# Optimization experiments

Measured on AMD Instinct MI355X. Metric: run time of the kernel, lower is better.

The kernel has to match this reference:

```python
import jax, jax.numpy as jnp
import numpy as np

NUM_HEADS = 16
HEAD_DIM = 128
ROTARY_DIM = 32  # head_dim * rotary_pct(0.25)
ROPE_BASE = 10000.0
SCALE = HEAD_DIM ** -0.5


def _rotate_half(x):
    x1, x2 = jnp.split(x, 2, axis=-1)
    return jnp.concatenate((-x2, x1), axis=-1)


def _rope_tables(seq_len, dtype):
    inv_freq = 1.0 / (ROPE_BASE ** (jnp.arange(0, ROTARY_DIM, 2, dtype=jnp.float32) / ROTARY_DIM))
    freqs = jnp.arange(seq_len, dtype=jnp.float32)[:, None] * inv_freq[None, :]  # [S, rd/2]
    emb = jnp.concatenate((freqs, freqs), axis=-1)  # [S, rd]
    return jnp.cos(emb).astype(dtype), jnp.sin(emb).astype(dtype)


def setup_inputs() -> dict:
    key = jax.random.key(0)
    k1, k2, k3 = jax.random.split(key, 3)
    B, S, H = 2, 2048, 2048
    hidden_states = jax.random.normal(k1, (B, S, H), dtype=jnp.float32)
    attention_mask = jnp.zeros((B, 1, S, S), dtype=jnp.float32)
    Wqkv = jax.random.normal(k2, (H, 3 * H), dtype=jnp.float32) * (H ** -0.5)
    Wout = jax.random.normal(k3, (H, H), dtype=jnp.float32) * (H ** -0.5)
    return {"hidden_states": hidden_states, "attention_mask": attention_mask,
            "Wqkv": Wqkv, "Wout": Wout}


def reference(hidden_states, attention_mask, Wqkv, Wout):
    B, S, H = hidden_states.shape
    qkv = jnp.einsum('bsh,hk->bsk', hidden_states, Wqkv)  # [B,S,3H]
    q, k, v = jnp.split(qkv, 3, axis=-1)

    def to_heads(x):
        return x.reshape(B, S, NUM_HEADS, HEAD_DIM).transpose(0, 2, 1, 3)  # [B,nh,S,hd]

    q, k, v = to_heads(q), to_heads(k), to_heads(v)

    cos, sin = _rope_tables(S, hidden_states.dtype)  # [S, ROTARY_DIM]
    cos = cos[None, None, :, :]
    sin = sin[None, None, :, :]

    def rope(x):
        xr = x[..., :ROTARY_DIM]
        xr = xr * cos + _rotate_half(xr) * sin
        return jnp.concatenate((xr, x[..., ROTARY_DIM:]), axis=-1)

    q, k = rope(q), rope(k)

    scores = jnp.einsum('bhqd,bhkd->bhqk', q, k) * SCALE + attention_mask
    probs = jax.nn.softmax(scores, axis=-1)  # dropout p=0 -> identity
    ctx = jnp.einsum('bhqk,bhkd->bhqd', probs, v)
    ctx = ctx.transpose(0, 2, 1, 3).reshape(B, S, H)
    return jnp.einsum('bsh,ho->bso', ctx, Wout)
```

## Files before the change

### kernel.cpp

```cpp
#include <hip/hip_runtime.h>

typedef __attribute__((ext_vector_type(4))) float f32x4;
typedef __attribute__((ext_vector_type(16))) float f32x16;
typedef __attribute__((ext_vector_type(8))) short s16x8;
typedef __attribute__((ext_vector_type(4))) unsigned short u16x4;
typedef __attribute__((ext_vector_type(8))) unsigned short u16x8;

#define DEVINL __device__ __forceinline__

constexpr int Bb = 2;
constexpr int Ss = 2048;
constexpr int Hh = 2048;
constexpr int NH = 16;
constexpr int HD = 128;
constexpr float ATT_SCALE = 0.08838834764831845f;
constexpr float CEXP = ATT_SCALE * 1.44269504089f;
constexpr float INV_SCALE = 11.313708498984761f;
constexpr float RAW_THR = 90.50966799f;

DEVINL unsigned short f2bf(float f) {
    unsigned u = __float_as_uint(f);
    u += 0x7FFFu + ((u >> 16) & 1u);
    return (unsigned short)(u >> 16);
}
DEVINL float bf2f(unsigned short h) { return __uint_as_float(((unsigned)h) << 16); }
DEVINL float fexp2(float x) { return __builtin_amdgcn_exp2f(x); }

DEVINL void gl16(const void* g, void* l) {
    __builtin_amdgcn_global_load_lds((const __attribute__((address_space(1))) void*)g,
                                     (__attribute__((address_space(3))) void*)l, 16, 0, 0);
}

__global__ void scan_mask_k(const float* __restrict__ m, int* __restrict__ flag) {
    size_t i = ((size_t)blockIdx.x * 256 + threadIdx.x) * 4;
    f32x4 v = *(const f32x4*)(m + i);
    int any = (v[0] != 0.f) || (v[1] != 0.f) || (v[2] != 0.f) || (v[3] != 0.f);
    if (__any(any)) { if ((threadIdx.x & 63) == 0) atomicOr(flag, 1); }
}

__global__ void convH_k(const float* __restrict__ x, unsigned short* __restrict__ y) {
    size_t i = (size_t)blockIdx.x * 256 + threadIdx.x;
    f32x4 a = *(const f32x4*)(x + i * 8);
    f32x4 b = *(const f32x4*)(x + i * 8 + 4);
    u16x8 o;
    o[0] = f2bf(a[0]); o[1] = f2bf(a[1]); o[2] = f2bf(a[2]); o[3] = f2bf(a[3]);
    o[4] = f2bf(b[0]); o[5] = f2bf(b[1]); o[6] = f2bf(b[2]); o[7] = f2bf(b[3]);
    *(u16x8*)(y + i * 8) = o;
}

__global__ void convT_k(const float* __restrict__ W, unsigned short* __restrict__ Wt,
                        int R, int C) {
    __shared__ float tile[32][33];
    int c0 = blockIdx.x * 32, r0 = blockIdx.y * 32;
    int t = threadIdx.x;
    int rr = t >> 3, cc = (t & 7) * 4;
    f32x4 v = *(const f32x4*)(W + (size_t)(r0 + rr) * C + c0 + cc);
    tile[rr][cc + 0] = v[0]; tile[rr][cc + 1] = v[1];
    tile[rr][cc + 2] = v[2]; tile[rr][cc + 3] = v[3];
    __syncthreads();
    u16x4 o;
    o[0] = f2bf(tile[cc + 0][rr]); o[1] = f2bf(tile[cc + 1][rr]);
    o[2] = f2bf(tile[cc + 2][rr]); o[3] = f2bf(tile[cc + 3][rr]);
    *(u16x4*)(Wt + (size_t)(c0 + rr) * R + r0 + cc) = o;
}

template<int MODE>
__global__ __launch_bounds__(512, 2)
void gemm128x256_k(const unsigned short* __restrict__ A, const unsigned short* __restrict__ Bt,
                   float* __restrict__ Cf, unsigned short* __restrict__ Cb,
                   unsigned short* __restrict__ VtOut,
                   int M, int N, int K, int rm, int rn, int snx) {
    __shared__ char lds[98304];
    int t = threadIdx.x, w = t >> 6, ln = t & 63, lr = ln & 15, lg = ln >> 4;
    int wm = w >> 2, wn = w & 3;
    int f = blockIdx.x;
    int xcd = f & 7, i0 = f >> 3;
    int mb = (xcd / snx) * rm + i0 % rm;
    int nb = (xcd % snx) * rn + i0 / rm;
    int m0 = mb * 128, n0 = nb * 256;
    const char* Ab = (const char*)A;
    const char* Bbp = (const char*)Bt;

    f32x4 acc[4][4];
#pragma unroll
    for (int i = 0; i < 4; ++i)
#pragma unroll
        for (int j = 0; j < 4; ++j) { acc[i][j][0] = 0.f; acc[i][j][1] = 0.f; acc[i][j][2] = 0.f; acc[i][j][3] = 0.f; }

    auto STGA = [&](int sbuf, int skh, int kt) {
        int row = t >> 2, c = t & 3;
        int cs = c ^ ((row >> 1) & 3);
        gl16(Ab + ((size_t)(m0 + row) * K + kt * 64 + skh * 32) * 2 + cs * 16,
             lds + sbuf * 49152 + skh * 8192 + t * 16);
    };
    auto STGB = [&](int sbuf, int skh, int kt) {
#pragma unroll
        for (int rr = 0; rr < 2; ++rr) {
            int ci = rr * 512 + t;
            int row = ci >> 2, c = ci & 3;
            int cs = c ^ ((row >> 1) & 3);
            gl16(Bbp + ((size_t)(n0 + row) * K + kt * 64 + skh * 32) * 2 + cs * 16,
                 lds + sbuf * 49152 + 16384 + skh * 16384 + ci * 16);
        }
    };

#define PH128(buf, kh, sbuf, skh, st)                                             \
  {                                                                               \
    const char* Ap = lds + (buf) * 49152 + (kh) * 8192;                           \
    const char* Bp = lds + (buf) * 49152 + 16384 + (kh) * 16384;                  \
    s16x8 af[4], bfr[4];                                                          \
    _Pragma("unroll")                                                             \
    for (int i = 0; i < 4; ++i) {                                                 \
      int row = wm * 64 + i * 16 + lr;                                            \
      af[i] = *(const s16x8*)(Ap + row * 64 + ((lg ^ ((row >> 1) & 3)) * 16));    \
    }                                                                             \
    _Pragma("unroll")                                                             \
    for (int j = 0; j < 4; ++j) {                                                 \
      int row = wn * 64 + j * 16 + lr;                                            \
      bfr[j] = *(const s16x8*)(Bp + row * 64 + ((lg ^ ((row >> 1) & 3)) * 16));   \
    }                                                                             \
    STGA(sbuf, skh, st); STGB(sbuf, skh, st);                                     \
    __builtin_amdgcn_s_barrier();                                                 \
    asm volatile("s_waitcnt lgkmcnt(0)" ::: "memory");                            \
    __builtin_amdgcn_s_setprio(1);                                                \
    _Pragma("unroll")                                                             \
    for (int i = 0; i < 4; ++i)                                                   \
      _Pragma("unroll")                                                           \
      for (int j = 0; j < 4; ++j)                                                 \
        acc[i][j] = __builtin_amdgcn_mfma_f32_16x16x32_bf16(af[i], bfr[j],        \
                                                            acc[i][j], 0, 0, 0); \
    __builtin_amdgcn_s_setprio(0);                                                \
    asm volatile("s_waitcnt vmcnt(6)" ::: "memory");                              \
    __builtin_amdgcn_s_barrier();                                                 \
  }

    const int NT = K >> 6;
    STGA(0, 0, 0); STGB(0, 0, 0);
    STGA(0, 1, 0); STGB(0, 1, 0);
    STGA(1, 0, 1); STGB(1, 0, 1);
    asm volatile("s_waitcnt vmcnt(3)" ::: "memory");
    __builtin_amdgcn_s_barrier();

    for (int it = 0; it < (NT >> 1); ++it) {
        int e = it * 2;
        int e2 = (e + 2 < NT) ? e + 2 : e;
        int e3 = (e + 3 < NT) ? e + 3 : e + 1;
        PH128(0, 0,  1, 1, e + 1)
        PH128(0, 1,  0, 0, e2)
        PH128(1, 0,  0, 1, e2)
        PH128(1, 1,  1, 0, e3)
    }
    asm volatile("s_waitcnt vmcnt(0)" ::: "memory");
#undef PH128

    if (MODE == 0 && n0 >= 4096) {
#pragma unroll
        for (int i = 0; i < 4; ++i)
#pragma unroll
            for (int j = 0; j < 4; ++j) {
                int vcol = n0 - 4096 + wn * 64 + j * 16 + lr;
                int h = vcol >> 7, d = vcol & 127;
                int gr = m0 + wm * 64 + i * 16 + lg * 4;
                int bb = gr >> 11, si = gr & 2047;
                u16x4 o;
                o[0] = f2bf(acc[i][j][0]); o[1] = f2bf(acc[i][j][1]);
                o[2] = f2bf(acc[i][j][2]); o[3] = f2bf(acc[i][j][3]);
                *(u16x4*)(VtOut + ((size_t)(bb * 16 + h) * 128 + d) * 2048 + si) = o;
            }
        return;
    }

    if (MODE == 0 && (wn & 1) == 0) {
        float invf = fexp2((float)lr * -0.83048202372f);
#pragma unroll
        for (int i = 0; i < 4; ++i)
#pragma unroll
            for (int r = 0; r < 4; ++r) {
                int srow = (m0 + wm * 64 + i * 16 + lg * 4 + r) & (Ss - 1);
                float sn, cs;
                sincosf((float)srow * invf, &sn, &cs);
                float x1 = acc[i][0][r], x2 = acc[i][1][r];
                acc[i][0][r] = x1 * cs - x2 * sn;
                acc[i][1][r] = x2 * cs + x1 * sn;
            }
    }

#pragma unroll
    for (int i = 0; i < 4; ++i)
#pragma unroll
        for (int j = 0; j < 4; ++j)
#pragma unroll
            for (int r = 0; r < 4; ++r) {
                int gr = m0 + wm * 64 + i * 16 + lg * 4 + r;
                int gc = n0 + wn * 64 + j * 16 + lr;
                float vv = acc[i][j][r];
                if (MODE == 1) Cf[(size_t)gr * N + gc] = vv;
                else           Cb[(size_t)gr * N + gc] = f2bf(vv);
            }
}

__global__ __launch_bounds__(512)
void attn_k(const unsigned short* __restrict__ qkv, const unsigned short* __restrict__ Vt,
            const float* __restrict__ mask, unsigned short* __restrict__ ctxb,
            const int* __restrict__ flag) {
    __shared__ char ldsK[2][16384];
    __shared__ char ldsV[2][16384];
    __shared__ unsigned short ldsP[8][2048];
    int f = blockIdx.x;
    int swzb = (f & 7) * 32 + (f >> 3);
    int bh = swzb >> 3, qt = swzb & 7;
    int b = bh >> 4, h = bh & 15;
    int t = threadIdx.x, w = t >> 6, ln = t & 63;
    int q5 = ln & 31, lg5 = ln >> 5;
    int useMask = *flag;
    int qb = qt * 256 + w * 32;
    const char* qkvB = (const char*)qkv;
    const char* VtB = (const char*)Vt;

    auto STAGE = [&](int buf, int kk0s) {
#pragma unroll
        for (int c = 0; c < 2; ++c) {
            int ci = c * 512 + t;
            int krow = ci >> 4, kcb = (ci & 15) << 4;
            gl16(qkvB + (((size_t)(b * Ss + kk0s + krow)) * 6144 + 2048 + h * 128) * 2 + (kcb ^ ((krow & 7) << 4)),
                 ldsK[buf] + ci * 16);
            int vrow = ci >> 3, vcb = (ci & 7) << 4;
            gl16(VtB + (((size_t)(bh * 128 + vrow)) * 2048 + kk0s) * 2 + (vcb ^ ((vrow & 7) << 4)),
                 ldsV[buf] + ci * 16);
        }
    };

    s16x8 qf[8];
    size_t qrow = ((size_t)(b * Ss + qb + q5)) * 6144 + h * 128;
#pragma unroll
    for (int dc = 0; dc < 8; ++dc) qf[dc] = *(const s16x8*)(qkv + qrow + dc * 16 + lg5 * 8);

    float mr = -3e38f, lsum = 0.f;
    f32x16 ctx[4];
#pragma unroll
    for (int dt = 0; dt < 4; ++dt)
#pragma unroll
        for (int r = 0; r < 16; ++r) ctx[dt][r] = 0.f;
    const float* mrow = mask + (size_t)b * Ss * Ss;

    STAGE(0, 0);
    asm volatile("s_waitcnt vmcnt(0)" ::: "memory");
    __builtin_amdgcn_s_barrier();

    for (int tix = 0; tix < 32; ++tix) {
        int kk0 = tix * 64;
        int cur = tix & 1;
        if (kk0 + 64 < Ss) STAGE(cur ^ 1, kk0 + 64);

        f32x16 st[2];
#pragma unroll
        for (int n = 0; n < 2; ++n) {
            f32x16 sacc;
#pragma unroll
            for (int r = 0; r < 16; ++r) sacc[r] = 0.f;
            int krow = n * 32 + q5;
            const char* kb = ldsK[cur] + krow * 256;
            int sw = krow & 7;
            __builtin_amdgcn_s_setprio(1);
#pragma unroll
            for (int dc = 0; dc < 8; ++dc) {
                s16x8 kf = *(const s16x8*)(kb + (((dc * 2 + lg5) ^ sw) << 4));
                sacc = __builtin_amdgcn_mfma_f32_32x32x16_bf16(kf, qf[dc], sacc, 0, 0, 0);
            }
            __builtin_amdgcn_s_setprio(0);
            st[n] = sacc;
        }
        if (useMask) {
#pragma unroll
            for (int n = 0; n < 2; ++n)
#pragma unroll
                for (int r = 0; r < 16; ++r) {
                    int kk = n * 32 + (r & 3) + 8 * (r >> 2) + 4 * lg5;
                    st[n][r] += mrow[(size_t)(qb + q5) * Ss + kk0 + kk] * INV_SCALE;
                }
        }
        float pmax = st[0][0];
#pragma unroll
        for (int n = 0; n < 2; ++n)
#pragma unroll
            for (int r = 0; r < 16; ++r) pmax = fmaxf(pmax, st[n][r]);
        pmax = fmaxf(pmax, __shfl_xor(pmax, 32));
        bool need = pmax > mr + RAW_THR;
        if (__any(need)) {
            float mn = fmaxf(mr, pmax);
            float al = fexp2((mr - mn) * CEXP);
            mr = mn;
            lsum *= al;
#pragma unroll
            for (int dt = 0; dt < 4; ++dt)
#pragma unroll
                for (int r = 0; r < 16; ++r)
                    ctx[dt][r] *= __shfl(al, (r & 3) + 8 * (r >> 2) + 4 * lg5);
        }
        float mC = mr * CEXP;
        float rs = 0.f;
#pragma unroll
        for (int n = 0; n < 2; ++n)
#pragma unroll
            for (int r = 0; r < 16; ++r) {
                float p = fexp2(st[n][r] * CEXP - mC);
                rs += p;
                st[n][r] = p;
            }
        rs += __shfl_xor(rs, 32);
        lsum += rs;
        char* pw = (char*)ldsP[w];
        int swq = q5 & 7;
#pragma unroll
        for (int n = 0; n < 2; ++n)
#pragma unroll
            for (int g = 0; g < 4; ++g) {
                u16x4 o;
                o[0] = f2bf(st[n][g * 4 + 0]); o[1] = f2bf(st[n][g * 4 + 1]);
                o[2] = f2bf(st[n][g * 4 + 2]); o[3] = f2bf(st[n][g * 4 + 3]);
                *(u16x4*)(pw + q5 * 128 + (((n * 4 + g) ^ swq) << 4) + lg5 * 8) = o;
            }
        asm volatile("s_waitcnt lgkmcnt(0)" ::: "memory");
        s16x8 pa[4];
#pragma unroll
        for (int c = 0; c < 4; ++c)
            pa[c] = *(const s16x8*)(pw + q5 * 128 + (((c * 2 + lg5) ^ swq) << 4));
#pragma unroll
        for (int dt = 0; dt < 4; ++dt) {
            int vrow = dt * 32 + q5;
            const char* vb = ldsV[cur] + vrow * 128;
            int swv = vrow & 7;
            __builtin_amdgcn_s_setprio(1);
#pragma unroll
            for (int c = 0; c < 4; ++c) {
                s16x8 vf = *(const s16x8*)(vb + (((c * 2 + lg5) ^ swv) << 4));
                ctx[dt] = __builtin_amdgcn_mfma_f32_32x32x16_bf16(pa[c], vf, ctx[dt], 0, 0, 0);
            }
            __builtin_amdgcn_s_setprio(0);
        }
        asm volatile("s_waitcnt vmcnt(0)" ::: "memory");
        __builtin_amdgcn_s_barrier();
    }
#pragma unroll
    for (int r = 0; r < 16; ++r) {
        int qr = (r & 3) + 8 * (r >> 2) + 4 * lg5;
        float li = 1.f / __shfl(lsum, qr);
        size_t base = ((size_t)(b * Ss + qb + qr)) * Hh + h * 128 + q5;
#pragma unroll
        for (int dt = 0; dt < 4; ++dt)
            ctxb[base + dt * 32] = f2bf(ctx[dt][r] * li);
    }
}

extern "C" void kernel_launch(void* const* d_in, const int* in_sizes, int n_in,
                              void* d_out, int out_size, void* d_ws, size_t ws_size,
                              hipStream_t stream) {
    (void)in_sizes; (void)n_in; (void)out_size; (void)ws_size;
    const float* hidden = (const float*)d_in[0];
    const float* mask   = (const float*)d_in[1];
    const float* Wqkv   = (const float*)d_in[2];
    const float* Wout   = (const float*)d_in[3];
    float* out = (float*)d_out;

    char* ws = (char*)d_ws;
    size_t off = 0;
    auto alloc = [&](size_t bytes) { char* p = ws + off; off += (bytes + 255) & ~(size_t)255; return p; };
    unsigned short* hbf   = (unsigned short*)alloc((size_t)8388608 * 2);
    unsigned short* wqkvT = (unsigned short*)alloc((size_t)12582912 * 2);
    unsigned short* woutT = (unsigned short*)alloc((size_t)4194304 * 2);
    unsigned short* qkv   = (unsigned short*)alloc((size_t)25165824 * 2);
    unsigned short* Vt    = (unsigned short*)alloc((size_t)8388608 * 2);
    int* flag             = (int*)alloc(256);
    unsigned short* ctx = hbf;

    hipMemsetAsync(flag, 0, 4, stream);
    scan_mask_k<<<8192, 256, 0, stream>>>(mask, flag);
    convH_k<<<4096, 256, 0, stream>>>(hidden, hbf);
    convT_k<<<dim3(192, 64), 256, 0, stream>>>(Wqkv, wqkvT, 2048, 6144);
    convT_k<<<dim3(64, 64), 256, 0, stream>>>(Wout, woutT, 2048, 2048);
    gemm128x256_k<0><<<768, 512, 0, stream>>>(hbf, wqkvT, nullptr, qkv, Vt,
                                              4096, 6144, 2048, 16, 6, 4);
    attn_k<<<256, 512, 0, stream>>>(qkv, Vt, mask, ctx, flag);
    gemm128x256_k<1><<<256, 512, 0, stream>>>(ctx, woutT, out, nullptr, nullptr,
                                              4096, 2048, 2048, 16, 2, 4);
}
```

Before: 296.3 us.

## Rebuild P operand via cross-lane shuffles instead of LDS round trip; widen K swizzle

The softmax probabilities are now repacked from the MFMA accumulator layout into the A-operand layout in registers, using __shfl_xor exchanges between lane halves. This replaces the write to the per-wave LDS P buffer, the lgkmcnt wait and the read back, and frees 32KB of shared memory. The K tile XOR swizzle also widens from 3 to 4 bits to cut LDS bank conflicts on the 256-byte rows. The shuffles themselves go through the LDS crossbar (ds_bpermute), so some of the saved latency may return.

```diff
diff --git a/kernel.cpp b/kernel.cpp
--- a/kernel.cpp
+++ b/kernel.cpp
@@ -205,7 +205,6 @@
             const int* __restrict__ flag) {
     __shared__ char ldsK[2][16384];
     __shared__ char ldsV[2][16384];
-    __shared__ unsigned short ldsP[8][2048];
     int f = blockIdx.x;
     int swzb = (f & 7) * 32 + (f >> 3);
     int bh = swzb >> 3, qt = swzb & 7;
@@ -222,7 +221,7 @@
         for (int c = 0; c < 2; ++c) {
             int ci = c * 512 + t;
             int krow = ci >> 4, kcb = (ci & 15) << 4;
-            gl16(qkvB + (((size_t)(b * Ss + kk0s + krow)) * 6144 + 2048 + h * 128) * 2 + (kcb ^ ((krow & 7) << 4)),
+            gl16(qkvB + (((size_t)(b * Ss + kk0s + krow)) * 6144 + 2048 + h * 128) * 2 + (kcb ^ ((krow & 15) << 4)),
                  ldsK[buf] + ci * 16);
             int vrow = ci >> 3, vcb = (ci & 7) << 4;
             gl16(VtB + (((size_t)(bh * 128 + vrow)) * 2048 + kk0s) * 2 + (vcb ^ ((vrow & 7) << 4)),
@@ -260,7 +259,7 @@
             for (int r = 0; r < 16; ++r) sacc[r] = 0.f;
             int krow = n * 32 + q5;
             const char* kb = ldsK[cur] + krow * 256;
-            int sw = krow & 7;
+            int sw = krow & 15;
             __builtin_amdgcn_s_setprio(1);
 #pragma unroll
             for (int dc = 0; dc < 8; ++dc) {
@@ -309,22 +308,26 @@
             }
         rs += __shfl_xor(rs, 32);
         lsum += rs;
-        char* pw = (char*)ldsP[w];
-        int swq = q5 & 7;
-#pragma unroll
-        for (int n = 0; n < 2; ++n)
-#pragma unroll
-            for (int g = 0; g < 4; ++g) {
-                u16x4 o;
-                o[0] = f2bf(st[n][g * 4 + 0]); o[1] = f2bf(st[n][g * 4 + 1]);
-                o[2] = f2bf(st[n][g * 4 + 2]); o[3] = f2bf(st[n][g * 4 + 3]);
-                *(u16x4*)(pw + q5 * 128 + (((n * 4 + g) ^ swq) << 4) + lg5 * 8) = o;
-            }
-        asm volatile("s_waitcnt lgkmcnt(0)" ::: "memory");
-        s16x8 pa[4];
-#pragma unroll
-        for (int c = 0; c < 4; ++c)
-            pa[c] = *(const s16x8*)(pw + q5 * 128 + (((c * 2 + lg5) ^ swq) << 4));
+        s16x8 paf[4];
+#pragma unroll
+        for (int c = 0; c < 4; ++c) {
+            const f32x16 sv = st[c >> 1];
+            const int cc = (c & 1) * 8;
+            unsigned loA = (unsigned)f2bf(sv[cc + 0]) | ((unsigned)f2bf(sv[cc + 1]) << 16);
+            unsigned loB = (unsigned)f2bf(sv[cc + 2]) | ((unsigned)f2bf(sv[cc + 3]) << 16);
+            unsigned hiA = (unsigned)f2bf(sv[cc + 4]) | ((unsigned)f2bf(sv[cc + 5]) << 16);
+            unsigned hiB = (unsigned)f2bf(sv[cc + 6]) | ((unsigned)f2bf(sv[cc + 7]) << 16);
+            unsigned sendA = lg5 ? loA : hiA;
+            unsigned sendB = lg5 ? loB : hiB;
+            unsigned recvA = (unsigned)__shfl_xor((int)sendA, 32);
+            unsigned recvB = (unsigned)__shfl_xor((int)sendB, 32);
+            union { s16x8 v; unsigned u[4]; } pu;
+            pu.u[0] = lg5 ? recvA : loA;
+            pu.u[1] = lg5 ? recvB : loB;
+            pu.u[2] = lg5 ? hiA : recvA;
+            pu.u[3] = lg5 ? hiB : recvB;
+            paf[c] = pu.v;
+        }
 #pragma unroll
         for (int dt = 0; dt < 4; ++dt) {
             int vrow = dt * 32 + q5;
@@ -334,7 +337,7 @@
 #pragma unroll
             for (int c = 0; c < 4; ++c) {
                 s16x8 vf = *(const s16x8*)(vb + (((c * 2 + lg5) ^ swv) << 4));
-                ctx[dt] = __builtin_amdgcn_mfma_f32_32x32x16_bf16(pa[c], vf, ctx[dt], 0, 0, 0);
+                ctx[dt] = __builtin_amdgcn_mfma_f32_32x32x16_bf16(paf[c], vf, ctx[dt], 0, 0, 0);
             }
             __builtin_amdgcn_s_setprio(0);
         }
```

After: 297.5 us. Within noise of the previous version (+0.4%).
